# Optimization experiments

Hardware: AMD Instinct MI355X
Metric: run time of the kernel (lower is better)

## Reference

```python
import jax, jax.numpy as jnp
import numpy as np

N_QUBITS = 8
N_CYCLES = 4
N_GATES = 10
MEAS_QUBITS = (3, 7)
BATCH = 16384


def _apply_ry_batched(state, angles, w):
    # angles: [B] per-example RY angle on wire w. state: [B,2,...,2]
    half = angles * 0.5
    c = jnp.cos(half).astype(jnp.complex64)
    s = jnp.sin(half).astype(jnp.complex64)
    U = jnp.stack([jnp.stack([c, -s], -1), jnp.stack([s, c], -1)], -2)  # [B,2,2]
    st = jnp.moveaxis(state, w + 1, -1)
    st = jnp.einsum('bij,b...j->b...i', U, st)
    return jnp.moveaxis(st, -1, w + 1)


def _apply_cnot(state, c, t):
    st = jnp.moveaxis(state, (c + 1, t + 1), (-2, -1))
    st = jnp.concatenate([st[..., 0:1, :], st[..., 1:2, ::-1]], axis=-2)
    return jnp.moveaxis(st, (-2, -1), (c + 1, t + 1))


def _apply_crx(state, theta, c, t):
    # CRX: RX(theta) on target when control=1 (torchquantum convention)
    half = theta * 0.5
    co = jnp.cos(half).astype(jnp.complex64)
    si = (-1j * jnp.sin(half)).astype(jnp.complex64)
    st = jnp.moveaxis(state, (c + 1, t + 1), (-2, -1))
    s1 = st[..., 1, :]
    s1 = jnp.stack([co * s1[..., 0] + si * s1[..., 1],
                    si * s1[..., 0] + co * s1[..., 1]], -1)
    st = jnp.concatenate([st[..., 0:1, :], s1[..., None, :]], axis=-2)
    return jnp.moveaxis(st, (-2, -1), (c + 1, t + 1))


def _expval_z(probs, w):
    axes = tuple(a for a in range(1, N_QUBITS + 1) if a != w + 1)
    m = jnp.sum(probs, axis=axes)  # [B,2]
    return m[:, 0] - m[:, 1]


def _forward(x, crx_theta, w1, b1, w2, b2):
    B = x.shape[0]
    state = jnp.zeros((B, 2 ** N_QUBITS), jnp.complex64).at[:, 0].set(1.0)
    state = state.reshape((B,) + (2,) * N_QUBITS)
    # encoding ansatz: per cycle, RY(x[:,cyc,q]) on each qubit + CNOT ring
    for cyc in range(N_CYCLES):
        for q in range(N_QUBITS):
            state = _apply_ry_batched(state, x[:, cyc, q], q)
        for q in range(N_QUBITS):
            state = _apply_cnot(state, q, (q + 1) % N_QUBITS)
    # trainable CRX layer
    for i in range(N_GATES):
        state = _apply_crx(state, crx_theta[i], i % N_QUBITS, (i + 1) % N_QUBITS)
    probs = jnp.abs(state) ** 2  # real, [B,2,...,2]
    feats = jnp.stack([_expval_z(probs, q) for q in MEAS_QUBITS], -1)  # [B,2]
    h = jnp.tanh(feats @ w1.T + b1)
    return jax.nn.sigmoid(h @ w2.T + b2)  # [B,1]


def setup_inputs() -> dict:
    key = jax.random.key(0)
    ks = jax.random.split(key, 6)
    x = jax.random.normal(ks[0], (BATCH, N_CYCLES, N_QUBITS), jnp.float32)
    crx_theta = jax.random.normal(ks[1], (N_GATES,), jnp.float32) * 0.1
    w1 = jax.random.normal(ks[2], (10, 2), jnp.float32) * (1.0 / np.sqrt(2.0))
    b1 = jnp.zeros((10,), jnp.float32)
    w2 = jax.random.normal(ks[3], (1, 10), jnp.float32) * (1.0 / np.sqrt(10.0))
    b2 = jnp.zeros((1,), jnp.float32)
    return {"x": x, "crx_theta": crx_theta, "w1": w1, "b1": b1, "w2": w2, "b2": b2}


def reference(x, crx_theta, w1, b1, w2, b2):
    return _forward(x, crx_theta, w1, b1, w2, b2)
```

## Files before the change

### kernel.cpp

```cpp
#include <hip/hip_runtime.h>
#include <math.h>


#define RLF(v, i) __int_as_float(__builtin_amdgcn_readlane(__float_as_int(v), (i)))
#define BPF(a, v) __int_as_float(__builtin_amdgcn_ds_bpermute((a), __float_as_int(v)))
#define DPPF(v, ctrl) __uint_as_float((unsigned)__builtin_amdgcn_update_dpp( \
    0, (int)__float_as_uint(v), (ctrl), 0xf, 0xf, true))
#define PX1(v)  DPPF((v), 0xB1)
#define PX2(v)  DPPF((v), 0x4E)
#define PX4(v)  DPPF(DPPF((v), 0x141), 0x1B)
#define PX8(v)  DPPF((v), 0x128)
#define PX16(v) BPF(a16, (v))
#define PX32(v) BPF(a32, (v))

__global__ __launch_bounds__(256, 8) void vqcnn_wave(
    const float* __restrict__ x,
    const float* __restrict__ crx_theta,
    const float* __restrict__ w1,
    const float* __restrict__ b1,
    const float* __restrict__ w2,
    const float* __restrict__ b2,
    float* __restrict__ out)
{
    const int lane = threadIdx.x & 63;
    const int b    = blockIdx.x * 4 + (threadIdx.x >> 6);

    float cv, sv;
    {
        float ang = 0.0f;
        if (lane < 32)      ang = x[b * 32 + lane];
        else if (lane < 42) ang = crx_theta[lane - 32];
        __sincosf(0.5f * ang, &sv, &cv);
    }

    const int a16 = (lane ^ 16) << 2;
    const int a32 = (lane ^ 32) << 2;
    const int g4  = (lane ^ (lane >> 1)) << 2;
    const int g4b = g4 ^ (48 << 2);
    const bool l0 = (lane & 1) != 0;

    float v0, v1, v2, v3;
    {
        float L = (lane & 32) ? RLF(sv, 0) : RLF(cv, 0);
        L *= (lane & 16) ? RLF(sv, 1) : RLF(cv, 1);
        L *= (lane &  8) ? RLF(sv, 2) : RLF(cv, 2);
        L *= (lane &  4) ? RLF(sv, 3) : RLF(cv, 3);
        L *= (lane &  2) ? RLF(sv, 4) : RLF(cv, 4);
        L *= (lane &  1) ? RLF(sv, 5) : RLF(cv, 5);
        const float c6 = RLF(cv, 6), s6 = RLF(sv, 6);
        const float c7 = RLF(cv, 7), s7 = RLF(sv, 7);
        const float Lc6 = L * c6, Ls6 = L * s6;
        v0 = Lc6 * c7; v1 = Lc6 * s7; v2 = Ls6 * c7; v3 = Ls6 * s7;
    }
#define RING() {                                                             \
    const float t0a = BPF(g4,  v0), t0b = BPF(g4,  v2);                      \
    const float t1a = BPF(g4b, v1), t1b = BPF(g4b, v3);                      \
    const float t2a = BPF(g4,  v3), t2b = BPF(g4,  v1);                      \
    const float t3a = BPF(g4b, v2), t3b = BPF(g4b, v0);                      \
    v0 = l0 ? t0b : t0a;  v1 = l0 ? t1b : t1a;                               \
    v2 = l0 ? t2b : t2a;  v3 = l0 ? t3b : t3a; }
    RING()

#define RY_G(ia, mask, PART) {                                               \
    const float c = RLF(cv, (ia)), s = RLF(sv, (ia));                        \
    const float ss = (lane & (mask)) ? s : -s;                               \
    const float p0 = PART(v0), p1 = PART(v1);                                \
    const float p2 = PART(v2), p3 = PART(v3);                                \
    v0 = fmaf(ss, p0, c * v0); v1 = fmaf(ss, p1, c * v1);                    \
    v2 = fmaf(ss, p2, c * v2); v3 = fmaf(ss, p3, c * v3); }

#define RY_SLOT1(ia) {                                                       \
    const float c = RLF(cv, (ia)), s = RLF(sv, (ia));                        \
    const float n0 = c*v0 - s*v2, n2 = s*v0 + c*v2;                          \
    const float n1 = c*v1 - s*v3, n3 = s*v1 + c*v3;                          \
    v0 = n0; v1 = n1; v2 = n2; v3 = n3; }

#define RY_SLOT0(ia) {                                                       \
    const float c = RLF(cv, (ia)), s = RLF(sv, (ia));                        \
    const float n0 = c*v0 - s*v1, n1 = s*v0 + c*v1;                          \
    const float n2 = c*v2 - s*v3, n3 = s*v2 + c*v3;                          \
    v0 = n0; v1 = n1; v2 = n2; v3 = n3; }

    #pragma unroll
    for (int cyc = 1; cyc < 4; ++cyc) {
        const int base = cyc * 8;
        RY_G(base + 0, 32, PX32)
        RY_G(base + 1, 16, PX16)
        RY_G(base + 2,  8, PX8)
        RY_G(base + 3,  4, PX4)
        RY_G(base + 4,  2, PX2)
        RY_G(base + 5,  1, PX1)
        RY_SLOT1(base + 6)
        RY_SLOT0(base + 7)
        RING()
    }

    float r0 = v0, r1 = v1, r2 = v2, r3 = v3;
    float i0 = 0.f, i1 = 0.f, i2 = 0.f, i3 = 0.f;

#define CRX_G(gi, cmask, PART) {                                             \
    const float c = RLF(cv, 32 + (gi)), s = RLF(sv, 32 + (gi));              \
    const bool ct = (lane & (cmask)) != 0;                                   \
    float pr, pi, nr, ni;                                                    \
    pr = PART(r0); pi = PART(i0);                                            \
    nr = c*r0 + s*pi; ni = c*i0 - s*pr; r0 = ct?nr:r0; i0 = ct?ni:i0;        \
    pr = PART(r1); pi = PART(i1);                                            \
    nr = c*r1 + s*pi; ni = c*i1 - s*pr; r1 = ct?nr:r1; i1 = ct?ni:i1;        \
    pr = PART(r2); pi = PART(i2);                                            \
    nr = c*r2 + s*pi; ni = c*i2 - s*pr; r2 = ct?nr:r2; i2 = ct?ni:i2;        \
    pr = PART(r3); pi = PART(i3);                                            \
    nr = c*r3 + s*pi; ni = c*i3 - s*pr; r3 = ct?nr:r3; i3 = ct?ni:i3; }

    CRX_G(0, 32, PX16)
    CRX_G(1, 16, PX8)
    CRX_G(2,  8, PX4)
    CRX_G(3,  4, PX2)
    CRX_G(4,  2, PX1)
    {
        const float c = RLF(cv, 37), s = RLF(sv, 37);
        const float nr0 = c*r0 + s*i2, ni0 = c*i0 - s*r2;
        const float nr2 = c*r2 + s*i0, ni2 = c*i2 - s*r0;
        const float nr1 = c*r1 + s*i3, ni1 = c*i1 - s*r3;
        const float nr3 = c*r3 + s*i1, ni3 = c*i3 - s*r1;
        r0 = l0?nr0:r0; i0 = l0?ni0:i0; r1 = l0?nr1:r1; i1 = l0?ni1:i1;
        r2 = l0?nr2:r2; i2 = l0?ni2:i2; r3 = l0?nr3:r3; i3 = l0?ni3:i3;
    }
    {
        const float c = RLF(cv, 38), s = RLF(sv, 38);
        const float nr2 = c*r2 + s*i3, ni2 = c*i2 - s*r3;
        const float nr3 = c*r3 + s*i2, ni3 = c*i3 - s*r2;
        r2 = nr2; i2 = ni2; r3 = nr3; i3 = ni3;
    }
    {
        const float c = RLF(cv, 39), s = RLF(sv, 39);
        const float pr1 = PX32(r1), pi1 = PX32(i1);
        const float pr3 = PX32(r3), pi3 = PX32(i3);
        const float nr1 = c*r1 + s*pi1, ni1 = c*i1 - s*pr1;
        const float nr3 = c*r3 + s*pi3, ni3 = c*i3 - s*pr3;
        r1 = nr1; i1 = ni1; r3 = nr3; i3 = ni3;
    }
    CRX_G(8, 32, PX16)
    CRX_G(9, 16, PX8)

    const float p0 = r0*r0 + i0*i0, p1 = r1*r1 + i1*i1;
    const float p2 = r2*r2 + i2*i2, p3 = r3*r3 + i3*i3;
    float vq7 = (p0 + p2) - (p1 + p3);
    float vq3 = (lane & 4) ? -(p0 + p1 + p2 + p3) : (p0 + p1 + p2 + p3);
    vq3 += PX1(vq3);   vq7 += PX1(vq7);
    vq3 += PX2(vq3);   vq7 += PX2(vq7);
    vq3 += PX4(vq3);   vq7 += PX4(vq7);
    vq3 += PX8(vq3);   vq7 += PX8(vq7);
    vq3 += PX16(vq3);  vq7 += PX16(vq7);
    vq3 += PX32(vq3);  vq7 += PX32(vq7);

    float wa = 0.f, wb = 0.f, bb = 0.f, wc = 0.f;
    if (lane < 10) {
        wa = w1[2 * lane];
        wb = w1[2 * lane + 1];
        bb = b1[lane];
        wc = w2[lane];
    }
    const float z = fmaf(wa, vq3, fmaf(wb, vq7, bb));
    const float e = __expf(2.0f * z);
    const float h = 1.0f - 2.0f * __builtin_amdgcn_rcpf(e + 1.0f);
    float acc = wc * h;
    acc += PX1(acc);
    acc += PX2(acc);
    acc += PX4(acc);
    acc += PX8(acc);
    if (lane == 0)
        out[b] = __builtin_amdgcn_rcpf(1.0f + __expf(-(acc + b2[0])));
}

extern "C" void kernel_launch(void* const* d_in, const int* in_sizes, int n_in,
                              void* d_out, int out_size, void* d_ws, size_t ws_size,
                              hipStream_t stream) {
    const float* x         = (const float*)d_in[0];
    const float* crx_theta = (const float*)d_in[1];
    const float* w1        = (const float*)d_in[2];
    const float* b1        = (const float*)d_in[3];
    const float* w2        = (const float*)d_in[4];
    const float* b2        = (const float*)d_in[5];
    float* out = (float*)d_out;

    const int B = in_sizes[0] / 32;
    vqcnn_wave<<<B / 4, 256, 0, stream>>>(x, crx_theta, w1, b1, w2, b2, out);
}
```

Before: 83.47 us.

## Process two batch samples per wavefront using packed float2 math

Each wavefront now simulates two batch examples at once, holding their state in float2 vectors so the arithmetic can map to packed FP32 instructions (v_pk_fma/v_pk_mul) on CDNA. The grid is halved to match. The aim is to cut per-sample instruction issue and amortise readlane and lane-index overhead across two samples. In exchange, register use roughly doubles and cross-lane permutes stay scalar, so DPP and bpermute traffic per wave doubles. This may lower occupancy or leave the kernel bound on LDS permute throughput.

```diff
diff --git a/kernel.cpp b/kernel.cpp
--- a/kernel.cpp
+++ b/kernel.cpp
@@ -1,17 +1,28 @@
 #include <hip/hip_runtime.h>
 #include <math.h>
 
+
+typedef float f2 __attribute__((ext_vector_type(2)));
 
 #define RLF(v, i) __int_as_float(__builtin_amdgcn_readlane(__float_as_int(v), (i)))
 #define BPF(a, v) __int_as_float(__builtin_amdgcn_ds_bpermute((a), __float_as_int(v)))
 #define DPPF(v, ctrl) __uint_as_float((unsigned)__builtin_amdgcn_update_dpp( \
     0, (int)__float_as_uint(v), (ctrl), 0xf, 0xf, true))
-#define PX1(v)  DPPF((v), 0xB1)
-#define PX2(v)  DPPF((v), 0x4E)
-#define PX4(v)  DPPF(DPPF((v), 0x141), 0x1B)
-#define PX8(v)  DPPF((v), 0x128)
-#define PX16(v) BPF(a16, (v))
-#define PX32(v) BPF(a32, (v))
+
+__device__ __forceinline__ f2 mk2(float a, float b) { f2 r; r.x = a; r.y = b; return r; }
+
+#define PX1S(v)  DPPF((v), 0xB1)
+#define PX2S(v)  DPPF((v), 0x4E)
+#define PX4S(v)  DPPF(DPPF((v), 0x141), 0x1B)
+#define PX8S(v)  DPPF((v), 0x128)
+
+#define PX1(v)  mk2(PX1S((v).x), PX1S((v).y))
+#define PX2(v)  mk2(PX2S((v).x), PX2S((v).y))
+#define PX4(v)  mk2(PX4S((v).x), PX4S((v).y))
+#define PX8(v)  mk2(PX8S((v).x), PX8S((v).y))
+#define PX16(v) mk2(BPF(a16, (v).x), BPF(a16, (v).y))
+#define PX32(v) mk2(BPF(a32, (v).x), BPF(a32, (v).y))
+#define FMA2(a, b, c) __builtin_elementwise_fma((a), (b), (c))
 
 __global__ __launch_bounds__(256, 8) void vqcnn_wave(
     const float* __restrict__ x,
@@ -23,14 +34,20 @@
     float* __restrict__ out)
 {
     const int lane = threadIdx.x & 63;
-    const int b    = blockIdx.x * 4 + (threadIdx.x >> 6);
-
-    float cv, sv;
-    {
-        float ang = 0.0f;
-        if (lane < 32)      ang = x[b * 32 + lane];
-        else if (lane < 42) ang = crx_theta[lane - 32];
-        __sincosf(0.5f * ang, &sv, &cv);
+    const int bA   = blockIdx.x * 8 + (threadIdx.x >> 6) * 2;
+    const int bB   = bA + 1;
+
+    float cvA, svA, cvB, svB;
+    {
+        float angA = 0.0f, angB = 0.0f;
+        if (lane < 32) {
+            angA = x[bA * 32 + lane];
+            angB = x[bB * 32 + lane];
+        } else if (lane < 42) {
+            angA = angB = crx_theta[lane - 32];
+        }
+        __sincosf(0.5f * angA, &svA, &cvA);
+        __sincosf(0.5f * angB, &svB, &cvB);
     }
 
     const int a16 = (lane ^ 16) << 2;
@@ -39,47 +56,53 @@
     const int g4b = g4 ^ (48 << 2);
     const bool l0 = (lane & 1) != 0;
 
-    float v0, v1, v2, v3;
-    {
-        float L = (lane & 32) ? RLF(sv, 0) : RLF(cv, 0);
-        L *= (lane & 16) ? RLF(sv, 1) : RLF(cv, 1);
-        L *= (lane &  8) ? RLF(sv, 2) : RLF(cv, 2);
-        L *= (lane &  4) ? RLF(sv, 3) : RLF(cv, 3);
-        L *= (lane &  2) ? RLF(sv, 4) : RLF(cv, 4);
-        L *= (lane &  1) ? RLF(sv, 5) : RLF(cv, 5);
-        const float c6 = RLF(cv, 6), s6 = RLF(sv, 6);
-        const float c7 = RLF(cv, 7), s7 = RLF(sv, 7);
-        const float Lc6 = L * c6, Ls6 = L * s6;
-        v0 = Lc6 * c7; v1 = Lc6 * s7; v2 = Ls6 * c7; v3 = Ls6 * s7;
-    }
+#define RL2C(i) mk2(RLF(cvA, (i)), RLF(cvB, (i)))
+#define RL2S(i) mk2(RLF(svA, (i)), RLF(svB, (i)))
+
+    f2 vv0, vv1, vv2, vv3;
+    {
+#define SEL0(bit, i) ((lane & (bit)) ? RL2S(i) : RL2C(i))
+        f2 L = SEL0(32, 0) * SEL0(16, 1);
+        L = L * SEL0(8, 2);
+        L = L * SEL0(4, 3);
+        L = L * SEL0(2, 4);
+        L = L * SEL0(1, 5);
+        const f2 c6 = RL2C(6), s6 = RL2S(6);
+        const f2 c7 = RL2C(7), s7 = RL2S(7);
+        const f2 Lc6 = L * c6, Ls6 = L * s6;
+        vv0 = Lc6 * c7; vv1 = Lc6 * s7; vv2 = Ls6 * c7; vv3 = Ls6 * s7;
+    }
+
 #define RING() {                                                             \
-    const float t0a = BPF(g4,  v0), t0b = BPF(g4,  v2);                      \
-    const float t1a = BPF(g4b, v1), t1b = BPF(g4b, v3);                      \
-    const float t2a = BPF(g4,  v3), t2b = BPF(g4,  v1);                      \
-    const float t3a = BPF(g4b, v2), t3b = BPF(g4b, v0);                      \
-    v0 = l0 ? t0b : t0a;  v1 = l0 ? t1b : t1a;                               \
-    v2 = l0 ? t2b : t2a;  v3 = l0 ? t3b : t3a; }
+    const f2 t0a = PXG(vv0), t0b = PXG(vv2);                                 \
+    const f2 t1a = PXGB(vv1), t1b = PXGB(vv3);                               \
+    const f2 t2a = PXG(vv3), t2b = PXG(vv1);                                 \
+    const f2 t3a = PXGB(vv2), t3b = PXGB(vv0);                               \
+    vv0 = l0 ? t0b : t0a;  vv1 = l0 ? t1b : t1a;                             \
+    vv2 = l0 ? t2b : t2a;  vv3 = l0 ? t3b : t3a; }
+#define PXG(v)  mk2(BPF(g4,  (v).x), BPF(g4,  (v).y))
+#define PXGB(v) mk2(BPF(g4b, (v).x), BPF(g4b, (v).y))
     RING()
 
 #define RY_G(ia, mask, PART) {                                               \
-    const float c = RLF(cv, (ia)), s = RLF(sv, (ia));                        \
-    const float ss = (lane & (mask)) ? s : -s;                               \
-    const float p0 = PART(v0), p1 = PART(v1);                                \
-    const float p2 = PART(v2), p3 = PART(v3);                                \
-    v0 = fmaf(ss, p0, c * v0); v1 = fmaf(ss, p1, c * v1);                    \
-    v2 = fmaf(ss, p2, c * v2); v3 = fmaf(ss, p3, c * v3); }
+    const f2 c = RL2C(ia), s = RL2S(ia);                                     \
+    const f2 ss = (lane & (mask)) ? s : -s;                                  \
+    const f2 p0 = PART(vv0), p1 = PART(vv1);                                 \
+    const f2 p2 = PART(vv2), p3 = PART(vv3);                                 \
+    vv0 = FMA2(ss, p0, c * vv0); vv1 = FMA2(ss, p1, c * vv1);                \
+    vv2 = FMA2(ss, p2, c * vv2); vv3 = FMA2(ss, p3, c * vv3); }
 
 #define RY_SLOT1(ia) {                                                       \
-    const float c = RLF(cv, (ia)), s = RLF(sv, (ia));                        \
-    const float n0 = c*v0 - s*v2, n2 = s*v0 + c*v2;                          \
-    const float n1 = c*v1 - s*v3, n3 = s*v1 + c*v3;                          \
-    v0 = n0; v1 = n1; v2 = n2; v3 = n3; }
+    const f2 c = RL2C(ia), s = RL2S(ia);                                     \
+    const f2 n0 = c*vv0 - s*vv2, n2 = FMA2(s, vv0, c*vv2);                   \
+    const f2 n1 = c*vv1 - s*vv3, n3 = FMA2(s, vv1, c*vv3);                   \
+    vv0 = n0; vv1 = n1; vv2 = n2; vv3 = n3; }
 
 #define RY_SLOT0(ia) {                                                       \
-    const float c = RLF(cv, (ia)), s = RLF(sv, (ia));                        \
-    const float n0 = c*v0 - s*v1, n1 = s*v0 + c*v1;                          \
-    const float n2 = c*v2 - s*v3, n3 = s*v2 + c*v3;                          \
-    v0 = n0; v1 = n1; v2 = n2; v3 = n3; }
+    const f2 c = RL2C(ia), s = RL2S(ia);                                     \
+    const f2 n0 = c*vv0 - s*vv1, n1 = FMA2(s, vv0, c*vv1);                   \
+    const f2 n2 = c*vv2 - s*vv3, n3 = FMA2(s, vv2, c*vv3);                   \
+    vv0 = n0; vv1 = n1; vv2 = n2; vv3 = n3; }
 
     #pragma unroll
     for (int cyc = 1; cyc < 4; ++cyc) {
@@ -95,21 +118,25 @@
         RING()
     }
 
-    float r0 = v0, r1 = v1, r2 = v2, r3 = v3;
-    float i0 = 0.f, i1 = 0.f, i2 = 0.f, i3 = 0.f;
+    f2 rr0 = vv0, rr1 = vv1, rr2 = vv2, rr3 = vv3;
+    f2 ii0 = {0.f, 0.f}, ii1 = {0.f, 0.f}, ii2 = {0.f, 0.f}, ii3 = {0.f, 0.f};
 
 #define CRX_G(gi, cmask, PART) {                                             \
-    const float c = RLF(cv, 32 + (gi)), s = RLF(sv, 32 + (gi));              \
+    const f2 c = RL2C(32 + (gi)), s = RL2S(32 + (gi));                       \
     const bool ct = (lane & (cmask)) != 0;                                   \
-    float pr, pi, nr, ni;                                                    \
-    pr = PART(r0); pi = PART(i0);                                            \
-    nr = c*r0 + s*pi; ni = c*i0 - s*pr; r0 = ct?nr:r0; i0 = ct?ni:i0;        \
-    pr = PART(r1); pi = PART(i1);                                            \
-    nr = c*r1 + s*pi; ni = c*i1 - s*pr; r1 = ct?nr:r1; i1 = ct?ni:i1;        \
-    pr = PART(r2); pi = PART(i2);                                            \
-    nr = c*r2 + s*pi; ni = c*i2 - s*pr; r2 = ct?nr:r2; i2 = ct?ni:i2;        \
-    pr = PART(r3); pi = PART(i3);                                            \
-    nr = c*r3 + s*pi; ni = c*i3 - s*pr; r3 = ct?nr:r3; i3 = ct?ni:i3; }
+    f2 pr, pi, nr, ni;                                                       \
+    pr = PART(rr0); pi = PART(ii0);                                          \
+    nr = FMA2(s, pi, c*rr0); ni = c*ii0 - s*pr;                              \
+    rr0 = ct?nr:rr0; ii0 = ct?ni:ii0;                                        \
+    pr = PART(rr1); pi = PART(ii1);                                          \
+    nr = FMA2(s, pi, c*rr1); ni = c*ii1 - s*pr;                              \
+    rr1 = ct?nr:rr1; ii1 = ct?ni:ii1;                                        \
+    pr = PART(rr2); pi = PART(ii2);                                          \
+    nr = FMA2(s, pi, c*rr2); ni = c*ii2 - s*pr;                              \
+    rr2 = ct?nr:rr2; ii2 = ct?ni:ii2;                                        \
+    pr = PART(rr3); pi = PART(ii3);                                          \
+    nr = FMA2(s, pi, c*rr3); ni = c*ii3 - s*pr;                              \
+    rr3 = ct?nr:rr3; ii3 = ct?ni:ii3; }
 
     CRX_G(0, 32, PX16)
     CRX_G(1, 16, PX8)
@@ -117,41 +144,42 @@
     CRX_G(3,  4, PX2)
     CRX_G(4,  2, PX1)
     {
-        const float c = RLF(cv, 37), s = RLF(sv, 37);
-        const float nr0 = c*r0 + s*i2, ni0 = c*i0 - s*r2;
-        const float nr2 = c*r2 + s*i0, ni2 = c*i2 - s*r0;
-        const float nr1 = c*r1 + s*i3, ni1 = c*i1 - s*r3;
-        const float nr3 = c*r3 + s*i1, ni3 = c*i3 - s*r1;
-        r0 = l0?nr0:r0; i0 = l0?ni0:i0; r1 = l0?nr1:r1; i1 = l0?ni1:i1;
-        r2 = l0?nr2:r2; i2 = l0?ni2:i2; r3 = l0?nr3:r3; i3 = l0?ni3:i3;
-    }
-    {
-        const float c = RLF(cv, 38), s = RLF(sv, 38);
-        const float nr2 = c*r2 + s*i3, ni2 = c*i2 - s*r3;
-        const float nr3 = c*r3 + s*i2, ni3 = c*i3 - s*r2;
-        r2 = nr2; i2 = ni2; r3 = nr3; i3 = ni3;
-    }
-    {
-        const float c = RLF(cv, 39), s = RLF(sv, 39);
-        const float pr1 = PX32(r1), pi1 = PX32(i1);
-        const float pr3 = PX32(r3), pi3 = PX32(i3);
-        const float nr1 = c*r1 + s*pi1, ni1 = c*i1 - s*pr1;
-        const float nr3 = c*r3 + s*pi3, ni3 = c*i3 - s*pr3;
-        r1 = nr1; i1 = ni1; r3 = nr3; i3 = ni3;
+        const f2 c = RL2C(37), s = RL2S(37);
+        const f2 nr0 = FMA2(s, ii2, c*rr0), ni0 = c*ii0 - s*rr2;
+        const f2 nr2 = FMA2(s, ii0, c*rr2), ni2 = c*ii2 - s*rr0;
+        const f2 nr1 = FMA2(s, ii3, c*rr1), ni1 = c*ii1 - s*rr3;
+        const f2 nr3 = FMA2(s, ii1, c*rr3), ni3 = c*ii3 - s*rr1;
+        rr0 = l0?nr0:rr0; ii0 = l0?ni0:ii0; rr1 = l0?nr1:rr1; ii1 = l0?ni1:ii1;
+        rr2 = l0?nr2:rr2; ii2 = l0?ni2:ii2; rr3 = l0?nr3:rr3; ii3 = l0?ni3:ii3;
+    }
+    {
+        const f2 c = RL2C(38), s = RL2S(38);
+        const f2 nr2 = FMA2(s, ii3, c*rr2), ni2 = c*ii2 - s*rr3;
+        const f2 nr3 = FMA2(s, ii2, c*rr3), ni3 = c*ii3 - s*rr2;
+        rr2 = nr2; ii2 = ni2; rr3 = nr3; ii3 = ni3;
+    }
+    {
+        const f2 c = RL2C(39), s = RL2S(39);
+        const f2 pr1 = PX32(rr1), pi1 = PX32(ii1);
+        const f2 pr3 = PX32(rr3), pi3 = PX32(ii3);
+        const f2 nr1 = FMA2(s, pi1, c*rr1), ni1 = c*ii1 - s*pr1;
+        const f2 nr3 = FMA2(s, pi3, c*rr3), ni3 = c*ii3 - s*pr3;
+        rr1 = nr1; ii1 = ni1; rr3 = nr3; ii3 = ni3;
     }
     CRX_G(8, 32, PX16)
     CRX_G(9, 16, PX8)
 
-    const float p0 = r0*r0 + i0*i0, p1 = r1*r1 + i1*i1;
-    const float p2 = r2*r2 + i2*i2, p3 = r3*r3 + i3*i3;
-    float vq7 = (p0 + p2) - (p1 + p3);
-    float vq3 = (lane & 4) ? -(p0 + p1 + p2 + p3) : (p0 + p1 + p2 + p3);
-    vq3 += PX1(vq3);   vq7 += PX1(vq7);
-    vq3 += PX2(vq3);   vq7 += PX2(vq7);
-    vq3 += PX4(vq3);   vq7 += PX4(vq7);
-    vq3 += PX8(vq3);   vq7 += PX8(vq7);
-    vq3 += PX16(vq3);  vq7 += PX16(vq7);
-    vq3 += PX32(vq3);  vq7 += PX32(vq7);
+    const f2 p0 = FMA2(rr0, rr0, ii0*ii0), p1 = FMA2(rr1, rr1, ii1*ii1);
+    const f2 p2 = FMA2(rr2, rr2, ii2*ii2), p3 = FMA2(rr3, rr3, ii3*ii3);
+    const f2 sum = (p0 + p1) + (p2 + p3);
+    f2 vq7 = (p0 + p2) - (p1 + p3);
+    f2 vq3 = (lane & 4) ? -sum : sum;
+    vq3 = vq3 + PX1(vq3);   vq7 = vq7 + PX1(vq7);
+    vq3 = vq3 + PX2(vq3);   vq7 = vq7 + PX2(vq7);
+    vq3 = vq3 + PX4(vq3);   vq7 = vq7 + PX4(vq7);
+    vq3 = vq3 + PX8(vq3);   vq7 = vq7 + PX8(vq7);
+    vq3 = vq3 + PX16(vq3);  vq7 = vq7 + PX16(vq7);
+    vq3 = vq3 + PX32(vq3);  vq7 = vq7 + PX32(vq7);
 
     float wa = 0.f, wb = 0.f, bb = 0.f, wc = 0.f;
     if (lane < 10) {
@@ -160,16 +188,20 @@
         bb = b1[lane];
         wc = w2[lane];
     }
-    const float z = fmaf(wa, vq3, fmaf(wb, vq7, bb));
-    const float e = __expf(2.0f * z);
-    const float h = 1.0f - 2.0f * __builtin_amdgcn_rcpf(e + 1.0f);
-    float acc = wc * h;
-    acc += PX1(acc);
-    acc += PX2(acc);
-    acc += PX4(acc);
-    acc += PX8(acc);
-    if (lane == 0)
-        out[b] = __builtin_amdgcn_rcpf(1.0f + __expf(-(acc + b2[0])));
+    const f2 z = FMA2(mk2(wa, wa), vq3, FMA2(mk2(wb, wb), vq7, mk2(bb, bb)));
+    const f2 e = mk2(__expf(2.0f * z.x), __expf(2.0f * z.y));
+    const f2 h = mk2(1.0f - 2.0f * __builtin_amdgcn_rcpf(e.x + 1.0f),
+                     1.0f - 2.0f * __builtin_amdgcn_rcpf(e.y + 1.0f));
+    f2 acc = mk2(wc, wc) * h;
+    acc = acc + PX1(acc);
+    acc = acc + PX2(acc);
+    acc = acc + PX4(acc);
+    acc = acc + PX8(acc);
+    if (lane == 0) {
+        const float bias = b2[0];
+        out[bA] = __builtin_amdgcn_rcpf(1.0f + __expf(-(acc.x + bias)));
+        out[bB] = __builtin_amdgcn_rcpf(1.0f + __expf(-(acc.y + bias)));
+    }
 }
 
 extern "C" void kernel_launch(void* const* d_in, const int* in_sizes, int n_in,
@@ -184,5 +216,5 @@
     float* out = (float*)d_out;
 
     const int B = in_sizes[0] / 32;
-    vqcnn_wave<<<B / 4, 256, 0, stream>>>(x, crx_theta, w1, b1, w2, b2, out);
+    vqcnn_wave<<<B / 8, 256, 0, stream>>>(x, crx_theta, w1, b1, w2, b2, out);
 }
```

After: 81.48 us. -2.4%, faster.
